# Optimization experiments

Hardware: AMD Instinct MI355X
Metric: run time of the kernel (lower is better)

## Reference

```python
import jax, jax.numpy as jnp
import numpy as np

SHIFT = 1  # fixed value of the randomized self.shift_direction (+1 or -1)


def _unfold_h3(t):
    """torch.nn.functional.unfold with kernel (3,1), padding (1,0),
    returned as (N, C, 3, H, W) patches (channel-major, kernel-minor order,
    matching torch's C*kh*kw channel layout)."""
    n, c, h, w = t.shape
    tp = jnp.pad(t, ((0, 0), (0, 0), (1, 1), (0, 0)))
    return jnp.stack([tp[:, :, k:k + h, :] for k in range(3)], axis=2)


def setup_inputs() -> dict:
    key = jax.random.key(0)
    kx, k1, k2 = jax.random.split(key, 3)
    x = jax.random.normal(kx, (128, 128, 56, 56), dtype=jnp.float32)
    w1 = jax.random.normal(k1, (64, 3, 4), dtype=jnp.float32)
    w2 = jax.random.normal(k2, (2, 3, 32), dtype=jnp.float32)
    return {"x": x, "w1": w1, "w2": w2}


def reference(x, w1, w2):
    # channel-group shift along H
    t = x.reshape(128, 64, 2, 56, 56)
    t = jnp.roll(t, SHIFT, axis=3)
    t = t.reshape(128, 128, 56, 56)
    # stage 1: vertical 3-tap patches + contraction over (k=64 channels, i=3 taps)
    p = _unfold_h3(t).reshape(128, 64, 2, 3, 56, 56)   # l k n i m o
    t4 = jnp.einsum('lknimo,kij->lnmoj', p, w1)        # (128, 2, 56, 56, 4)
    # stage 2: fold (n,m)->112 channels, 3-tap patches along o-dim, contract (i=2, k=3)
    t5 = t4.reshape(128, 112, 56, 4)
    p2 = _unfold_h3(t5).reshape(128, 2, 56, 3, 56, 4)  # l i m k n o
    t6 = jnp.einsum('limkno,ikj->lmnoj', p2, w2)       # (128, 56, 56, 4, 32)
    y = jnp.transpose(t6, (0, 1, 2, 4, 3)).reshape(128, 56, 56, 128)
    return jnp.transpose(y, (0, 3, 1, 2))              # (128, 128, 56, 56)
```

## Files before the change

### kernel.cpp

```cpp
#include <hip/hip_runtime.h>


__global__ __launch_bounds__(256) void stage1_kernel(
    const float* __restrict__ x, const float* __restrict__ w1,
    float* __restrict__ t4)
{
    const int bid  = (blockIdx.x & 7) * 49 + (blockIdx.x >> 3);
    const int item = bid * 256 + threadIdx.x;
    const int l  = item / 784;
    const int r  = item - l * 784;
    const int m  = r / 14;
    const int o0 = (r - m * 14) * 4;

    int   off[3];
    float vf[3];
#pragma unroll
    for (int t = 0; t < 3; ++t) {
        const int h = m + t - 1;
        vf[t] = (h >= 0 && h < 56) ? 1.0f : 0.0f;
        const int row = (h <= 0) ? 55 : (h - 1);
        off[t] = row * 56 + o0;
    }

    float acc[2][4][4] = {};
    const float* xl = x + (size_t)l * (128 * 3136);

    for (int k = 0; k < 64; ++k) {
        float w[3][4];
#pragma unroll
        for (int t = 0; t < 3; ++t)
#pragma unroll
            for (int j = 0; j < 4; ++j)
                w[t][j] = w1[(k * 3 + t) * 4 + j] * vf[t];

#pragma unroll
        for (int i2 = 0; i2 < 2; ++i2) {
            const float* xc = xl + (size_t)(2 * k + i2) * 3136;
#pragma unroll
            for (int t = 0; t < 3; ++t) {
                const float4 xv = *reinterpret_cast<const float4*>(xc + off[t]);
#pragma unroll
                for (int j = 0; j < 4; ++j) {
                    acc[i2][j][0] = fmaf(xv.x, w[t][j], acc[i2][j][0]);
                    acc[i2][j][1] = fmaf(xv.y, w[t][j], acc[i2][j][1]);
                    acc[i2][j][2] = fmaf(xv.z, w[t][j], acc[i2][j][2]);
                    acc[i2][j][3] = fmaf(xv.w, w[t][j], acc[i2][j][3]);
                }
            }
        }
    }

    float* tp = t4 + (size_t)l * (8 * 3136) + m * 56 + o0;
#pragma unroll
    for (int i2 = 0; i2 < 2; ++i2)
#pragma unroll
        for (int j = 0; j < 4; ++j) {
            const float4 v = make_float4(acc[i2][j][0], acc[i2][j][1],
                                         acc[i2][j][2], acc[i2][j][3]);
            *reinterpret_cast<float4*>(tp + (size_t)(i2 * 4 + j) * 3136) = v;
        }
}

__global__ __launch_bounds__(256) void stage2_kernel(
    const float* __restrict__ t4, const float* __restrict__ w2,
    float* __restrict__ out)
{
    const int l  = blockIdx.x >> 3;
    const int o4 = (blockIdx.x >> 1) & 3;
    const int mh = blockIdx.x & 1;

    __shared__ float lds[2][1568];
    const int tid = threadIdx.x;

    const float* p0 = t4 + ((size_t)l * 8 + 0 + o4) * 3136 + mh * 1568;
    const float* p1 = t4 + ((size_t)l * 8 + 4 + o4) * 3136 + mh * 1568;
    for (int t = tid; t < 784; t += 256) {
        const int i2 = (t >= 392);
        const int p4 = i2 ? t - 392 : t;
        const float4 v = *reinterpret_cast<const float4*>(
            (i2 ? p1 : p0) + (size_t)p4 * 4);
        *reinterpret_cast<float4*>(&lds[i2][p4 * 4]) = v;
    }
    __syncthreads();

    for (int ch = tid; ch < 392; ch += 256) {
        const int ml = ch / 14;
        const int n0 = (ch - ml * 14) * 4;
        const int m  = mh * 28 + ml;

        float tv[2][6];
#pragma unroll
        for (int i = 0; i < 2; ++i)
#pragma unroll
            for (int d = 0; d < 6; ++d) {
                const int nn = n0 - 1 + d;
                tv[i][d] = (nn >= 0 && nn < 56) ? lds[i][ml * 56 + nn] : 0.0f;
            }

        float* ob = out + ((size_t)l * 128 + o4) * 3136 + m * 56 + n0;
#pragma unroll
        for (int j = 0; j < 32; ++j) {
            float4 s = make_float4(0.f, 0.f, 0.f, 0.f);
#pragma unroll
            for (int i = 0; i < 2; ++i)
#pragma unroll
                for (int k = 0; k < 3; ++k) {
                    const float wv = w2[(i * 3 + k) * 32 + j];
                    s.x = fmaf(tv[i][k + 0], wv, s.x);
                    s.y = fmaf(tv[i][k + 1], wv, s.y);
                    s.z = fmaf(tv[i][k + 2], wv, s.z);
                    s.w = fmaf(tv[i][k + 3], wv, s.w);
                }
            *reinterpret_cast<float4*>(ob + (size_t)j * 4 * 3136) = s;
        }
    }
}

extern "C" void kernel_launch(void* const* d_in, const int* in_sizes, int n_in,
                              void* d_out, int out_size, void* d_ws, size_t ws_size,
                              hipStream_t stream)
{
    const float* x  = (const float*)d_in[0];
    const float* w1 = (const float*)d_in[1];
    const float* w2 = (const float*)d_in[2];
    float* out = (float*)d_out;
    float* t4  = (float*)d_ws;

    stage1_kernel<<<dim3(392), dim3(256), 0, stream>>>(x, w1, t4);
    stage2_kernel<<<dim3(1024), dim3(256), 0, stream>>>(t4, w2, out);
}
```

Baseline: 439.4 us.

## Split stage1 channel reduction across four waves with LDS reduction

Stage1 now splits the 64-channel reduction across the four wavefronts of each block, 16 channels per wave, so each block handles 64 output positions. The grid grows from 392 to 1568 blocks to fill the GPU's compute units. Partial sums from waves 1-3 go through shared memory and wave 0 adds them and writes the result. The added cost is a barrier, extra LDS traffic and fewer output positions per block.

```diff
diff --git a/kernel.cpp b/kernel.cpp
--- a/kernel.cpp
+++ b/kernel.cpp
@@ -5,12 +5,16 @@
     const float* __restrict__ x, const float* __restrict__ w1,
     float* __restrict__ t4)
 {
-    const int bid  = (blockIdx.x & 7) * 49 + (blockIdx.x >> 3);
-    const int item = bid * 256 + threadIdx.x;
-    const int l  = item / 784;
-    const int r  = item - l * 784;
-    const int m  = r / 14;
-    const int o0 = (r - m * 14) * 4;
+    const int bid   = ((int)blockIdx.x & 7) * 196 + ((int)blockIdx.x >> 3);
+    const int tid   = threadIdx.x;
+    const int chunk = tid & 63;
+    const int kg    = __builtin_amdgcn_readfirstlane(tid >> 6);
+
+    const int p4 = bid * 64 + chunk;
+    const int l  = p4 / 784;
+    const int rc = p4 - l * 784;
+    const int m  = rc / 14;
+    const int o0 = (rc - m * 14) * 4;
 
     int   off[3];
     float vf[3];
@@ -24,8 +28,11 @@
 
     float acc[2][4][4] = {};
     const float* xl = x + (size_t)l * (128 * 3136);
+    const int k0 = kg * 16;
 
-    for (int k = 0; k < 64; ++k) {
+#pragma unroll 4
+    for (int kk = 0; kk < 16; ++kk) {
+        const int k = k0 + kk;
         float w[3][4];
 #pragma unroll
         for (int t = 0; t < 3; ++t)
@@ -50,15 +57,35 @@
         }
     }
 
-    float* tp = t4 + (size_t)l * (8 * 3136) + m * 56 + o0;
+    __shared__ float4 lds[3 * 8 * 64];
+    if (kg != 0) {
 #pragma unroll
-    for (int i2 = 0; i2 < 2; ++i2)
+        for (int i2 = 0; i2 < 2; ++i2)
 #pragma unroll
-        for (int j = 0; j < 4; ++j) {
-            const float4 v = make_float4(acc[i2][j][0], acc[i2][j][1],
-                                         acc[i2][j][2], acc[i2][j][3]);
-            *reinterpret_cast<float4*>(tp + (size_t)(i2 * 4 + j) * 3136) = v;
-        }
+            for (int j = 0; j < 4; ++j)
+                lds[(((kg - 1) * 8) + (i2 * 4 + j)) * 64 + chunk] =
+                    make_float4(acc[i2][j][0], acc[i2][j][1],
+                                acc[i2][j][2], acc[i2][j][3]);
+    }
+    __syncthreads();
+
+    if (kg == 0) {
+        float* tp = t4 + (size_t)l * (8 * 3136) + m * 56 + o0;
+#pragma unroll
+        for (int i2 = 0; i2 < 2; ++i2)
+#pragma unroll
+            for (int j = 0; j < 4; ++j) {
+                const int out = i2 * 4 + j;
+                float4 s = make_float4(acc[i2][j][0], acc[i2][j][1],
+                                       acc[i2][j][2], acc[i2][j][3]);
+#pragma unroll
+                for (int g = 0; g < 3; ++g) {
+                    const float4 v = lds[(g * 8 + out) * 64 + chunk];
+                    s.x += v.x; s.y += v.y; s.z += v.z; s.w += v.w;
+                }
+                *reinterpret_cast<float4*>(tp + (size_t)out * 3136) = s;
+            }
+    }
 }
 
 __global__ __launch_bounds__(256) void stage2_kernel(
@@ -126,6 +153,6 @@
     float* out = (float*)d_out;
     float* t4  = (float*)d_ws;
 
-    stage1_kernel<<<dim3(392), dim3(256), 0, stream>>>(x, w1, t4);
+    stage1_kernel<<<dim3(1568), dim3(256), 0, stream>>>(x, w1, t4);
     stage2_kernel<<<dim3(1024), dim3(256), 0, stream>>>(t4, w2, out);
 }
```

Result: faster. 375.9 us (-14.4%).

## Stage input tiles through LDS with register prefetch and re-tile stage2 output

Applied to the files above, without the earlier changes.

Stage1 now assigns each block a 14-row slab of one image. It streams the 128 channels in groups of 8 through shared memory, prefetching the next group into registers, so the three vertical taps come from LDS instead of repeated global loads. Stage2 is re-tiled so each block handles two rows with a zero-padded LDS tile and weights cached in LDS. This removes the boundary branches and spreads output writes across many more blocks and threads. The cost is extra synchronisation, idle threads in stage1 (60 of 256 do no compute), and larger LDS use per block.

```diff
diff --git a/kernel.cpp b/kernel.cpp
--- a/kernel.cpp
+++ b/kernel.cpp
@@ -5,114 +5,164 @@
     const float* __restrict__ x, const float* __restrict__ w1,
     float* __restrict__ t4)
 {
-    const int bid  = (blockIdx.x & 7) * 49 + (blockIdx.x >> 3);
-    const int item = bid * 256 + threadIdx.x;
-    const int l  = item / 784;
-    const int r  = item - l * 784;
-    const int m  = r / 14;
-    const int o0 = (r - m * 14) * 4;
+    const int bid  = ((int)blockIdx.x & 7) * 64 + ((int)blockIdx.x >> 3);
+    const int l    = bid >> 2;
+    const int m0   = (bid & 3) * 14;
+    const int tid  = threadIdx.x;
 
-    int   off[3];
+    const int row = tid / 14;
+    const int nc  = tid - row * 14;
+    const bool is_comp = (tid < 196);
+
     float vf[3];
 #pragma unroll
     for (int t = 0; t < 3; ++t) {
-        const int h = m + t - 1;
+        const int h = m0 + row + t - 1;
         vf[t] = (h >= 0 && h < 56) ? 1.0f : 0.0f;
-        const int row = (h <= 0) ? 55 : (h - 1);
-        off[t] = row * 56 + o0;
+    }
+
+    __shared__ float xs[8 * 16 * 56];
+
+    int   g_off[7];
+    const float* xl = x + (size_t)l * (128 * 3136);
+#pragma unroll
+    for (int r = 0; r < 7; ++r) {
+        const int it  = tid + r * 256;
+        const int cc  = it / 224;
+        const int rem = it - cc * 224;
+        const int lr  = rem / 14;
+        const int nc4 = rem - lr * 14;
+        const int rr  = m0 - 1 + lr;
+        const int src = (rr <= 0) ? 55 : (rr - 1);
+        g_off[r] = cc * 3136 + src * 56 + nc4 * 4;
     }
 
     float acc[2][4][4] = {};
-    const float* xl = x + (size_t)l * (128 * 3136);
 
-    for (int k = 0; k < 64; ++k) {
-        float w[3][4];
+    float4 pre[7];
 #pragma unroll
-        for (int t = 0; t < 3; ++t)
+    for (int r = 0; r < 7; ++r)
+        pre[r] = *reinterpret_cast<const float4*>(xl + g_off[r]);
+
+    for (int b = 0; b < 16; ++b) {
 #pragma unroll
-            for (int j = 0; j < 4; ++j)
-                w[t][j] = w1[(k * 3 + t) * 4 + j] * vf[t];
+        for (int r = 0; r < 7; ++r)
+            *reinterpret_cast<float4*>(&xs[(tid + r * 256) * 4]) = pre[r];
 
+        if (b < 15) {
+            const float* xb = xl + (size_t)(b + 1) * 8 * 3136;
 #pragma unroll
-        for (int i2 = 0; i2 < 2; ++i2) {
-            const float* xc = xl + (size_t)(2 * k + i2) * 3136;
+            for (int r = 0; r < 7; ++r)
+                pre[r] = *reinterpret_cast<const float4*>(xb + g_off[r]);
+        }
+        __syncthreads();
+
+        if (is_comp) {
 #pragma unroll
-            for (int t = 0; t < 3; ++t) {
-                const float4 xv = *reinterpret_cast<const float4*>(xc + off[t]);
+            for (int cc = 0; cc < 8; ++cc) {
+                const int c  = b * 8 + cc;
+                const int k  = c >> 1;
+                const int i2 = c & 1;
+                float w[3][4];
 #pragma unroll
-                for (int j = 0; j < 4; ++j) {
-                    acc[i2][j][0] = fmaf(xv.x, w[t][j], acc[i2][j][0]);
-                    acc[i2][j][1] = fmaf(xv.y, w[t][j], acc[i2][j][1]);
-                    acc[i2][j][2] = fmaf(xv.z, w[t][j], acc[i2][j][2]);
-                    acc[i2][j][3] = fmaf(xv.w, w[t][j], acc[i2][j][3]);
+                for (int t = 0; t < 3; ++t)
+#pragma unroll
+                    for (int j = 0; j < 4; ++j)
+                        w[t][j] = w1[(k * 3 + t) * 4 + j] * vf[t];
+#pragma unroll
+                for (int t = 0; t < 3; ++t) {
+                    const float4 xv = *reinterpret_cast<const float4*>(
+                        &xs[((cc * 16 + row + t) * 56) + nc * 4]);
+#pragma unroll
+                    for (int j = 0; j < 4; ++j) {
+                        acc[i2][j][0] = fmaf(xv.x, w[t][j], acc[i2][j][0]);
+                        acc[i2][j][1] = fmaf(xv.y, w[t][j], acc[i2][j][1]);
+                        acc[i2][j][2] = fmaf(xv.z, w[t][j], acc[i2][j][2]);
+                        acc[i2][j][3] = fmaf(xv.w, w[t][j], acc[i2][j][3]);
+                    }
                 }
             }
         }
+        __syncthreads();
     }
 
-    float* tp = t4 + (size_t)l * (8 * 3136) + m * 56 + o0;
+    if (is_comp) {
+        float* tp = t4 + (size_t)l * (8 * 3136) + (m0 + row) * 56 + nc * 4;
 #pragma unroll
-    for (int i2 = 0; i2 < 2; ++i2)
+        for (int i2 = 0; i2 < 2; ++i2)
 #pragma unroll
-        for (int j = 0; j < 4; ++j) {
-            const float4 v = make_float4(acc[i2][j][0], acc[i2][j][1],
-                                         acc[i2][j][2], acc[i2][j][3]);
-            *reinterpret_cast<float4*>(tp + (size_t)(i2 * 4 + j) * 3136) = v;
-        }
+            for (int j = 0; j < 4; ++j) {
+                *reinterpret_cast<float4*>(tp + (size_t)(i2 * 4 + j) * 3136) =
+                    make_float4(acc[i2][j][0], acc[i2][j][1],
+                                acc[i2][j][2], acc[i2][j][3]);
+            }
+    }
 }
 
 __global__ __launch_bounds__(256) void stage2_kernel(
     const float* __restrict__ t4, const float* __restrict__ w2,
     float* __restrict__ out)
 {
-    const int l  = blockIdx.x >> 3;
-    const int o4 = (blockIdx.x >> 1) & 3;
-    const int mh = blockIdx.x & 1;
-
-    __shared__ float lds[2][1568];
+    const int bid = ((int)blockIdx.x & 7) * 448 + ((int)blockIdx.x >> 3);
+    const int l   = bid / 28;
+    const int m0  = (bid - l * 28) * 2;
     const int tid = threadIdx.x;
 
-    const float* p0 = t4 + ((size_t)l * 8 + 0 + o4) * 3136 + mh * 1568;
-    const float* p1 = t4 + ((size_t)l * 8 + 4 + o4) * 3136 + mh * 1568;
-    for (int t = tid; t < 784; t += 256) {
-        const int i2 = (t >= 392);
-        const int p4 = i2 ? t - 392 : t;
+    __shared__ float tl[8 * 2 * 64];
+    __shared__ float w2l[192];
+
+    if (tid < 192) w2l[tid] = w2[tid];
+    if (tid < 32) {
+        const int o  = tid >> 2;
+        const int rw = (tid >> 1) & 1;
+        const int cl = (tid & 1) ? 60 : 3;
+        tl[(o * 2 + rw) * 64 + cl] = 0.0f;
+    }
+    if (tid < 224) {
+        const int o   = tid / 28;
+        const int rem = tid - o * 28;
+        const int rw  = rem / 14;
+        const int nc  = rem - rw * 14;
         const float4 v = *reinterpret_cast<const float4*>(
-            (i2 ? p1 : p0) + (size_t)p4 * 4);
-        *reinterpret_cast<float4*>(&lds[i2][p4 * 4]) = v;
+            t4 + ((size_t)l * 8 + o) * 3136 + (m0 + rw) * 56 + nc * 4);
+        *reinterpret_cast<float4*>(&tl[(o * 2 + rw) * 64 + 4 + nc * 4]) = v;
     }
     __syncthreads();
 
-    for (int ch = tid; ch < 392; ch += 256) {
-        const int ml = ch / 14;
-        const int n0 = (ch - ml * 14) * 4;
-        const int m  = mh * 28 + ml;
+    const int o4 = tid >> 6;
+    const int ln = tid & 63;
+
+    float* ob = out + ((size_t)l * 128 + o4) * 3136 + m0 * 56;
+
+#pragma unroll 2
+    for (int r = 0; r < 14; ++r) {
+        const int task = r * 64 + ln;
+        const int j    = task / 28;
+        const int rem  = task - j * 28;
+        const int rw   = rem / 14;
+        const int nc   = rem - rw * 14;
 
         float tv[2][6];
 #pragma unroll
+        for (int i = 0; i < 2; ++i) {
+            const float* tb = &tl[((i * 4 + o4) * 2 + rw) * 64 + 3 + nc * 4];
+#pragma unroll
+            for (int d = 0; d < 6; ++d) tv[i][d] = tb[d];
+        }
+
+        float4 s = make_float4(0.f, 0.f, 0.f, 0.f);
+#pragma unroll
         for (int i = 0; i < 2; ++i)
 #pragma unroll
-            for (int d = 0; d < 6; ++d) {
-                const int nn = n0 - 1 + d;
-                tv[i][d] = (nn >= 0 && nn < 56) ? lds[i][ml * 56 + nn] : 0.0f;
+            for (int k = 0; k < 3; ++k) {
+                const float wv = w2l[(i * 3 + k) * 32 + j];
+                s.x = fmaf(tv[i][k + 0], wv, s.x);
+                s.y = fmaf(tv[i][k + 1], wv, s.y);
+                s.z = fmaf(tv[i][k + 2], wv, s.z);
+                s.w = fmaf(tv[i][k + 3], wv, s.w);
             }
-
-        float* ob = out + ((size_t)l * 128 + o4) * 3136 + m * 56 + n0;
-#pragma unroll
-        for (int j = 0; j < 32; ++j) {
-            float4 s = make_float4(0.f, 0.f, 0.f, 0.f);
-#pragma unroll
-            for (int i = 0; i < 2; ++i)
-#pragma unroll
-                for (int k = 0; k < 3; ++k) {
-                    const float wv = w2[(i * 3 + k) * 32 + j];
-                    s.x = fmaf(tv[i][k + 0], wv, s.x);
-                    s.y = fmaf(tv[i][k + 1], wv, s.y);
-                    s.z = fmaf(tv[i][k + 2], wv, s.z);
-                    s.w = fmaf(tv[i][k + 3], wv, s.w);
-                }
-            *reinterpret_cast<float4*>(ob + (size_t)j * 4 * 3136) = s;
-        }
+        *reinterpret_cast<float4*>(
+            ob + (size_t)(4 * j) * 3136 + rw * 56 + nc * 4) = s;
     }
 }
 
@@ -126,6 +176,6 @@
     float* out = (float*)d_out;
     float* t4  = (float*)d_ws;
 
-    stage1_kernel<<<dim3(392), dim3(256), 0, stream>>>(x, w1, t4);
-    stage2_kernel<<<dim3(1024), dim3(256), 0, stream>>>(t4, w2, out);
+    stage1_kernel<<<dim3(512), dim3(256), 0, stream>>>(x, w1, t4);
+    stage2_kernel<<<dim3(3584), dim3(256), 0, stream>>>(t4, w2, out);
 }
```

Result: faster. 403.0 us (-8.3%).
